# Optimization experiments

Hardware: AMD Instinct MI355X
Metric: run time of the kernel (lower is better)

## Reference

```python
import jax, jax.numpy as jnp
import numpy as np

D_IN = 1024
D_OUT = 1024
NUM_HEADS = 16
HEAD_DIM = D_OUT // NUM_HEADS


def setup_inputs() -> dict:
    key = jax.random.key(0)
    ks = jax.random.split(key, 6)
    s = 0.02
    x = jax.random.normal(ks[0], (2, 2048, D_IN), dtype=jnp.float32)
    wq = jax.random.normal(ks[1], (D_IN, D_OUT), dtype=jnp.float32) * s
    wk = jax.random.normal(ks[2], (D_IN, D_OUT), dtype=jnp.float32) * s
    wv = jax.random.normal(ks[3], (D_IN, D_OUT), dtype=jnp.float32) * s
    wo = jax.random.normal(ks[4], (D_OUT, D_OUT), dtype=jnp.float32) * s
    bo = jax.random.normal(ks[5], (D_OUT,), dtype=jnp.float32) * s
    return {"x": x, "wq": wq, "wk": wk, "wv": wv, "wo": wo, "bo": bo}


def reference(x, wq, wk, wv, wo, bo):
    B, S, _ = x.shape
    # QKV projections (no bias, qkv_bias=False)
    def split_heads(t):
        return t.reshape(B, S, NUM_HEADS, HEAD_DIM).transpose(0, 2, 1, 3)  # [B,H,S,Dh]
    q = split_heads(x @ wq)
    k = split_heads(x @ wk)
    v = split_heads(x @ wv)
    scores = jnp.einsum('bhqd,bhkd->bhqk', q, k) / np.sqrt(HEAD_DIM).astype(np.float32)
    causal = jnp.tril(jnp.ones((S, S), dtype=bool))  # [S,S]
    scores = jnp.where(causal[None, None], scores, -jnp.inf)
    attn = jax.nn.softmax(scores, axis=-1)  # dropout p=0.0 -> identity
    ctx = jnp.einsum('bhqk,bhkd->bhqd', attn, v)
    ctx = ctx.transpose(0, 2, 1, 3).reshape(B, S, D_OUT)
    return ctx @ wo + bo
```

## Files before the change

kernel.cpp:

```cpp
#include <hip/hip_runtime.h>

typedef short s16x8 __attribute__((ext_vector_type(8)));
typedef float f32x4 __attribute__((ext_vector_type(4)));
typedef float f32x16 __attribute__((ext_vector_type(16)));
typedef unsigned int u32;
typedef u32 u32x2 __attribute__((ext_vector_type(2)));
typedef u32 u32x4 __attribute__((ext_vector_type(4)));
typedef unsigned short u16;

#define MFMA16(a, b, c) __builtin_amdgcn_mfma_f32_16x16x32_bf16((a), (b), (c), 0, 0, 0)
#define MFMA32(a, b, c) __builtin_amdgcn_mfma_f32_32x32x16_bf16((a), (b), (c), 0, 0, 0)

__device__ __forceinline__ u16 f2bf(float f) {
  unsigned u = __builtin_bit_cast(unsigned, f);
  unsigned r = (u + 0x7FFFu + ((u >> 16) & 1u)) >> 16;
  return (u16)r;
}

__device__ __forceinline__ u32 pack2bf(float lo, float hi) {
  return (u32)f2bf(lo) | ((u32)f2bf(hi) << 16);
}

__device__ __forceinline__ u32 cvtpk(float lo, float hi) {
  u32 r;
  asm("v_cvt_pk_bf16_f32 %0, %1, %2" : "=v"(r) : "v"(lo), "v"(hi));
  return r;
}

__device__ __forceinline__ float bf2f(u32 lo16) {
  return __builtin_bit_cast(float, lo16 << 16);
}

__device__ __forceinline__ void gl_lds16(const u16* g, u16* s) {
  __builtin_amdgcn_global_load_lds(
      (const __attribute__((address_space(1))) void*)g,
      (__attribute__((address_space(3))) void*)s, 16, 0, 0);
}

__global__ __launch_bounds__(256) void cvt_bf16(const float* __restrict__ in,
                                                u16* __restrict__ out, int n4) {
  int i = blockIdx.x * 256 + threadIdx.x;
  if (i < n4) {
    float4 v = reinterpret_cast<const float4*>(in)[i];
    ushort4 o;
    o.x = f2bf(v.x); o.y = f2bf(v.y); o.z = f2bf(v.z); o.w = f2bf(v.w);
    reinterpret_cast<ushort4*>(out)[i] = o;
  }
}

__global__ __launch_bounds__(256) void transp4(const float* __restrict__ wq,
                                               const float* __restrict__ wk,
                                               const float* __restrict__ wv,
                                               const float* __restrict__ wo,
                                               u16* __restrict__ wqkvt,
                                               u16* __restrict__ wot, float qscale) {
  __shared__ float tile[64][65];
  int z = blockIdx.z;
  const float* W = (z == 0) ? wq : (z == 1) ? wk : (z == 2) ? wv : wo;
  u16* out = (z < 3) ? (wqkvt + z * 1048576) : wot;
  float sc = (z == 0) ? qscale : 1.0f;
  int n0 = blockIdx.x * 64, k0 = blockIdx.y * 64;
  int t = threadIdx.x;
#pragma unroll
  for (int i = 0; i < 16; i++) {
    int idx = t + i * 256;
    int r = idx >> 6, c = idx & 63;
    tile[r][c] = W[(k0 + r) * 1024 + (n0 + c)];
  }
  __syncthreads();
#pragma unroll
  for (int i = 0; i < 16; i++) {
    int idx = t + i * 256;
    int r = idx >> 6, c = idx & 63;
    out[(n0 + r) * 1024 + (k0 + c)] = f2bf(tile[c][r] * sc);
  }
}

template <int MODE>
__global__ __launch_bounds__(256) void gemm2(const u16* __restrict__ A,
                                             const u16* __restrict__ Bt,
                                             const float* __restrict__ bias,
                                             void* __restrict__ outp) {
  constexpr int K = 1024, NT = K / 32;
  __shared__ __align__(16) u16 As[2][128 * 32];
  __shared__ __align__(16) u16 Bs[2][128 * 32];
  int t = threadIdx.x, w = t >> 6, l = t & 63;
  int m0 = blockIdx.y * 128, n0 = blockIdx.x * 128;
  int wm = (w >> 1) * 64, wn = (w & 1) * 64;
  int g = l >> 4, ql = l & 15;

  f32x4 acc[4][4];
#pragma unroll
  for (int i = 0; i < 4; i++)
#pragma unroll
    for (int j = 0; j < 4; j++) acc[i][j] = f32x4{0.f, 0.f, 0.f, 0.f};

  int lrow = l >> 2, lcol = (l & 3) * 8;
  const u16* Ag0 = A + (m0 + 32 * w + lrow) * K + lcol;
  const u16* Bg0 = Bt + (n0 + 32 * w + lrow) * K + lcol;
  u16* Asw[2] = {&As[0][(32 * w) * 32], &As[1][(32 * w) * 32]};
  u16* Bsw[2] = {&Bs[0][(32 * w) * 32], &Bs[1][(32 * w) * 32]};

#define STAGE(buf, kt)                              \
  do {                                              \
    int k0_ = (kt) * 32;                            \
    gl_lds16(Ag0 + k0_, Asw[buf]);                  \
    gl_lds16(Ag0 + 16 * K + k0_, Asw[buf] + 512);   \
    gl_lds16(Bg0 + k0_, Bsw[buf]);                  \
    gl_lds16(Bg0 + 16 * K + k0_, Bsw[buf] + 512);   \
  } while (0)

#define COMPUTE(buf)                                                              \
  do {                                                                            \
    s16x8 af[4], bv[4];                                                           \
    _Pragma("unroll") for (int fm = 0; fm < 4; fm++)                              \
        af[fm] = *reinterpret_cast<const s16x8*>(                                 \
            &As[buf][(wm + fm * 16 + ql) * 32 + g * 8]);                          \
    _Pragma("unroll") for (int fn = 0; fn < 4; fn++)                              \
        bv[fn] = *reinterpret_cast<const s16x8*>(                                 \
            &Bs[buf][(wn + fn * 16 + ql) * 32 + g * 8]);                          \
    _Pragma("unroll") for (int fm = 0; fm < 4; fm++)                              \
        _Pragma("unroll") for (int fn = 0; fn < 4; fn++)                          \
            acc[fm][fn] = MFMA16(af[fm], bv[fn], acc[fm][fn]);                    \
  } while (0)

  STAGE(0, 0);
  __syncthreads();
  int cur = 0;
  for (int kt = 0; kt < NT - 1; kt++) {
    STAGE(cur ^ 1, kt + 1);
    COMPUTE(cur);
    __syncthreads();
    cur ^= 1;
  }
  COMPUTE(cur);
#undef STAGE
#undef COMPUTE

#pragma unroll
  for (int fm = 0; fm < 4; fm++)
#pragma unroll
    for (int fn = 0; fn < 4; fn++)
#pragma unroll
      for (int j = 0; j < 4; j++) {
        int m = m0 + wm + fm * 16 + g * 4 + j;
        int n = n0 + wn + fn * 16 + ql;
        float v = acc[fm][fn][j];
        if (MODE == 0) {
          int proj = n >> 10, nn = n & 1023;
          int bh = (m >> 11) * 16 + (nn >> 6);
          int hd = nn & 63, srow = m & 2047;
          u16* o = (u16*)outp + proj * 4194304;
          if (proj < 2) {
            o[(bh * 2048 + srow) * 64 + hd] = f2bf(v);
          } else {
            int sp = (srow & ~12) | ((srow & 4) << 1) | ((srow & 8) >> 1);
            o[(bh * 64 + hd) * 2048 + sp] = f2bf(v);
          }
        } else {
          ((float*)outp)[m * 1024 + n] = v + bias[n];
        }
      }
}

__global__ __launch_bounds__(512, 4) void attn_kernel(const u16* __restrict__ Q,
                                                      const u16* __restrict__ Kb,
                                                      const u16* __restrict__ Vt,
                                                      u16* __restrict__ Ctx,
                                                      u16* __restrict__ part_o,
                                                      float* __restrict__ part_l) {
  __shared__ __align__(16) u16 Kl[2][2048];
  __shared__ __align__(16) u16 Vl[2][2048];
  __shared__ __align__(16) u16 tl[8][32 * 68];
  int tid = threadIdx.x, w = tid >> 6, l = tid & 63;
  int lq = l & 31, h = l >> 5;

  int B = blockIdx.x;
  int head = (B & 7) + 8 * ((B >> 3) & 3);
  int u = B >> 5;
  const signed char QCv[16] = {3, 2, 4, 4, 6, 6, 6, 7, 7, 7, 7, 5, 5, 5, 1, 0};
  const signed char CKv[16] = {0, 0, 0, 1, 0, 1, 2, 0, 1, 2, 3, 0, 1, 2, 0, 0};
  int qc = QCv[u], ck = CKv[u];
  int t0, t1;
  if (qc == 4)      { t0 = ck * 20; t1 = t0 + 20; }
  else if (qc == 5) { t0 = ck * 16; t1 = t0 + 16; }
  else if (qc == 6) { t0 = (ck == 0) ? 0 : (ck == 1) ? 19 : 38;
                      t1 = (ck == 0) ? 19 : (ck == 1) ? 38 : 56; }
  else if (qc == 7) { t0 = ck * 16; t1 = t0 + 16; }
  else              { t0 = 0; t1 = (qc + 1) * 8; }
  int dtile = qc * 8 + w;
  int q0w = qc * 256 + w * 32;
  int q = q0w + lq;

  const u16* Qp = Q + (head * 2048 + q0w) * 64;
  const u16* Kp = Kb + head * 2048 * 64;
  const u16* Vp = Vt + head * 64 * 2048;

  s16x8 qf[4];
#pragma unroll
  for (int f = 0; f < 4; f++)
    qf[f] = *reinterpret_cast<const s16x8*>(Qp + lq * 64 + f * 16 + h * 8);

  const u16* gstage;
  int gstep, ldsoff;
  if (w < 4) {
    int row = w * 8 + (l >> 3);
    int c = (l & 7) ^ (row & 7);
    gstage = Kp + row * 64 + c * 8;
    gstep = 32 * 64;
    ldsoff = w * 512;
  } else {
    int lin = (w - 4) * 64 + l;
    int rp = lin >> 3, pos = lin & 7;
    int d = rp * 2 + (pos >> 2);
    int c = (pos & 3) ^ (rp & 3);
    gstage = Vp + d * 2048 + c * 8;
    gstep = 32;
    ldsoff = (w - 4) * 512;
  }

  f32x16 oacc[2];
#pragma unroll
  for (int dt = 0; dt < 2; dt++)
#pragma unroll
    for (int rr = 0; rr < 16; rr++) oacc[dt][rr] = 0.f;
  float lsum = 0.f;

#define STAGE(buf, kt)                                                    \
  gl_lds16(gstage + (kt) * gstep, ((w < 4) ? Kl[buf] : Vl[buf]) + ldsoff)

  STAGE(0, t0);
  __syncthreads();
  int cur = 0;

  for (int kt = t0; kt < t1; kt++) {
    if (kt + 1 < t1) STAGE(cur ^ 1, kt + 1);

    if (kt <= dtile) {
      s16x8 kc[4];
#pragma unroll
      for (int f = 0; f < 4; f++)
        kc[f] = *reinterpret_cast<const s16x8*>(
            &Kl[cur][lq * 64 + (((f * 2 + h) ^ (lq & 7)) * 8)]);

      f32x16 s;
#pragma unroll
      for (int rr = 0; rr < 16; rr++) s[rr] = 0.f;
      __builtin_amdgcn_s_setprio(1);
#pragma unroll
      for (int f = 0; f < 4; f++) s = MFMA32(kc[f], qf[f], s);
      __builtin_amdgcn_s_setprio(0);

      float p[16];
      if (kt == dtile) {
        int kb = kt * 32;
#pragma unroll
        for (int rr = 0; rr < 16; rr++) {
          int key = kb + (rr & 3) + 8 * (rr >> 2) + 4 * h;
          float e = exp2f(s[rr]);
          p[rr] = (key <= q) ? e : 0.f;
        }
      } else {
#pragma unroll
        for (int rr = 0; rr < 16; rr++) p[rr] = exp2f(s[rr]);
      }
#pragma unroll
      for (int rr = 0; rr < 16; rr++) lsum += p[rr];

      u32 pw[2][4];
#pragma unroll
      for (int kh = 0; kh < 2; kh++)
#pragma unroll
        for (int uu = 0; uu < 4; uu++)
          pw[kh][uu] = cvtpk(p[kh * 8 + 2 * uu], p[kh * 8 + 2 * uu + 1]);

      s16x8 vf[2][2];
#pragma unroll
      for (int dt = 0; dt < 2; dt++)
#pragma unroll
        for (int kh = 0; kh < 2; kh++) {
          int rp = dt * 16 + (lq >> 1);
          int soff = rp * 64 + (lq & 1) * 32 + (((kh * 2 + h) ^ (rp & 3)) * 8);
          vf[dt][kh] = *reinterpret_cast<const s16x8*>(&Vl[cur][soff]);
        }

      __builtin_amdgcn_s_setprio(1);
#pragma unroll
      for (int kh = 0; kh < 2; kh++) {
        s16x8 pf = __builtin_bit_cast(
            s16x8, u32x4{pw[kh][0], pw[kh][1], pw[kh][2], pw[kh][3]});
        oacc[0] = MFMA32(vf[0][kh], pf, oacc[0]);
        oacc[1] = MFMA32(vf[1][kh], pf, oacc[1]);
      }
      __builtin_amdgcn_s_setprio(0);
    }

    __syncthreads();
    cur ^= 1;
  }
#undef STAGE

  if (qc >= 4) {
    int base = (qc == 4) ? 0 : (qc == 5) ? 2 : (qc == 6) ? 5 : 8;
    int rec = head * 12 + base + ck;
    u32* po = reinterpret_cast<u32*>(part_o) + (size_t)rec * 8192 + w * 1024 + l * 16;
#pragma unroll
    for (int dt = 0; dt < 2; dt++)
#pragma unroll
      for (int i = 0; i < 8; i++)
        po[dt * 8 + i] = pack2bf(oacc[dt][2 * i], oacc[dt][2 * i + 1]);
    part_l[(size_t)rec * 512 + w * 64 + l] = lsum;
    return;
  }

  float ltot = lsum + __shfl_xor(lsum, 32);
  float invl = 1.0f / ltot;
  u16* myl = tl[w];
#pragma unroll
  for (int dt = 0; dt < 2; dt++)
#pragma unroll
    for (int i = 0; i < 8; i++) {
      int d = ((2 * i) & 3) + 8 * (i >> 1) + 4 * h + dt * 32;
      u32 pkv = pack2bf(oacc[dt][2 * i] * invl, oacc[dt][2 * i + 1] * invl);
      *reinterpret_cast<u32*>(myl + lq * 68 + d) = pkv;
    }

  int b = head >> 4, hh = head & 15;
  int gbase = b * 2048 + q0w;
#pragma unroll
  for (int i = 0; i < 8; i++) {
    int chunkk = i * 64 + l;
    int row = chunkk >> 4, col4 = (chunkk & 15) * 4;
    u32x2 v = *reinterpret_cast<const u32x2*>(myl + row * 68 + col4);
    *reinterpret_cast<u32x2*>(Ctx + (gbase + row) * 1024 + hh * 64 + col4) = v;
  }
}

__global__ __launch_bounds__(256) void attn_combine(const u16* __restrict__ part_o,
                                                    const float* __restrict__ part_l,
                                                    u16* __restrict__ Ctx) {
  __shared__ __align__(16) u16 tl[4][32 * 68];
  int wv = threadIdx.x >> 6, l = threadIdx.x & 63;
  int lq = l & 31, h = l >> 5;
  int unit = blockIdx.x * 4 + wv;
  int head = unit & 31, rest = unit >> 5;
  int qc = 4 + (rest >> 3), w = rest & 7;
  int nc = (qc == 4) ? 2 : (qc == 7) ? 4 : 3;
  int base = (qc == 4) ? 0 : (qc == 5) ? 2 : (qc == 6) ? 5 : 8;
  int rec0 = head * 12 + base;

  float lsum = 0.f;
  float of[32];
#pragma unroll
  for (int i = 0; i < 32; i++) of[i] = 0.f;
  for (int cc = 0; cc < nc; cc++) {
    int rec = rec0 + cc;
    lsum += part_l[(size_t)rec * 512 + w * 64 + l];
    const u32* po =
        reinterpret_cast<const u32*>(part_o) + (size_t)rec * 8192 + w * 1024 + l * 16;
#pragma unroll
    for (int uu = 0; uu < 16; uu++) {
      u32 a = po[uu];
      of[2 * uu] += bf2f(a & 0xFFFFu);
      of[2 * uu + 1] += bf2f(a >> 16);
    }
  }

  float ltot = lsum + __shfl_xor(lsum, 32);
  float invl = 1.0f / ltot;

  u16* myl = tl[wv];
#pragma unroll
  for (int dt = 0; dt < 2; dt++)
#pragma unroll
    for (int i = 0; i < 8; i++) {
      int uu = dt * 8 + i;
      int d = ((2 * i) & 3) + 8 * (i >> 1) + 4 * h + dt * 32;
      *reinterpret_cast<u32*>(myl + lq * 68 + d) =
          pack2bf(of[2 * uu] * invl, of[2 * uu + 1] * invl);
    }

  int b_ = head >> 4, hh = head & 15;
  int gbase = b_ * 2048 + qc * 256 + w * 32;
#pragma unroll
  for (int i = 0; i < 8; i++) {
    int chunkk = i * 64 + l;
    int row = chunkk >> 4, col4 = (chunkk & 15) * 4;
    u32x2 v = *reinterpret_cast<const u32x2*>(myl + row * 68 + col4);
    *reinterpret_cast<u32x2*>(Ctx + (gbase + row) * 1024 + hh * 64 + col4) = v;
  }
}

extern "C" void kernel_launch(void* const* d_in, const int* in_sizes, int n_in,
                              void* d_out, int out_size, void* d_ws, size_t ws_size,
                              hipStream_t stream) {
  const float* x = (const float*)d_in[0];
  const float* wq = (const float*)d_in[1];
  const float* wk = (const float*)d_in[2];
  const float* wv = (const float*)d_in[3];
  const float* wo = (const float*)d_in[4];
  const float* bo = (const float*)d_in[5];

  char* ws = (char*)d_ws;
  const size_t MB = 1 << 20;
  u16* xb    = (u16*)(ws + 0 * MB);
  u16* wqkvt = (u16*)(ws + 8 * MB);
  u16* wot   = (u16*)(ws + 14 * MB);
  u16* qkv   = (u16*)(ws + 16 * MB);
  u16* ctx   = (u16*)(ws + 40 * MB);
  u16* part_o   = (u16*)(ws + 0 * MB);
  float* part_l = (float*)(ws + 12582912);

  const float QSCALE = 0.125f * 1.44269504f;

  cvt_bf16<<<4096, 256, 0, stream>>>(x, xb, 1048576);
  transp4<<<dim3(16, 16, 4), 256, 0, stream>>>(wq, wk, wv, wo, wqkvt, wot, QSCALE);

  gemm2<0><<<dim3(24, 32), 256, 0, stream>>>(xb, wqkvt, nullptr, qkv);

  attn_kernel<<<512, 512, 0, stream>>>(qkv, qkv + 4194304, qkv + 8388608, ctx,
                                       part_o, part_l);
  attn_combine<<<256, 256, 0, stream>>>(part_o, part_l, ctx);

  gemm2<1><<<dim3(8, 32), 256, 0, stream>>>(ctx, wot, bo, d_out);
}
```

Measured before the change: 122.1 us.

## Triple-buffer 64-key stages with prefetch depth two in causal attention

Replaces the double-buffered 32-key K/V staging with a triple-buffered ring of 64-key stages, prefetching two stages ahead and waiting with explicit vmcnt counts plus raw s_barrier instead of __syncthreads. Each iteration processes two 32-key subtiles, which halves the number of barriers. The per-block split of key ranges is rebalanced and the block ordering reshuffled, and the shared memory is unified into one buffer that the epilogue staging area aliases. The aim is to hide global-load latency and cut synchronisation overhead, at the cost of more LDS per block (48 KB), which may lower occupancy, and of the fragility of hand-placed waitcnts.

Result: no change. 122.2 us (+0.1%).

```diff
diff --git a/kernel.cpp b/kernel.cpp
--- a/kernel.cpp
+++ b/kernel.cpp
@@ -169,25 +169,18 @@
                                                       u16* __restrict__ Ctx,
                                                       u16* __restrict__ part_o,
                                                       float* __restrict__ part_l) {
-  __shared__ __align__(16) u16 Kl[2][2048];
-  __shared__ __align__(16) u16 Vl[2][2048];
-  __shared__ __align__(16) u16 tl[8][32 * 68];
+  __shared__ __align__(16) u16 shm[24576];
   int tid = threadIdx.x, w = tid >> 6, l = tid & 63;
   int lq = l & 31, h = l >> 5;
 
   int B = blockIdx.x;
   int head = (B & 7) + 8 * ((B >> 3) & 3);
   int u = B >> 5;
-  const signed char QCv[16] = {3, 2, 4, 4, 6, 6, 6, 7, 7, 7, 7, 5, 5, 5, 1, 0};
-  const signed char CKv[16] = {0, 0, 0, 1, 0, 1, 2, 0, 1, 2, 3, 0, 1, 2, 0, 0};
-  int qc = QCv[u], ck = CKv[u];
-  int t0, t1;
-  if (qc == 4)      { t0 = ck * 20; t1 = t0 + 20; }
-  else if (qc == 5) { t0 = ck * 16; t1 = t0 + 16; }
-  else if (qc == 6) { t0 = (ck == 0) ? 0 : (ck == 1) ? 19 : 38;
-                      t1 = (ck == 0) ? 19 : (ck == 1) ? 38 : 56; }
-  else if (qc == 7) { t0 = ck * 16; t1 = t0 + 16; }
-  else              { t0 = 0; t1 = (qc + 1) * 8; }
+  const signed char QCp[16]  = {3, 2, 4, 4, 6, 6, 6, 5, 5, 5, 7, 7, 7, 7, 1, 0};
+  const signed char T0pv[16] = {0, 0, 0, 10, 0, 10, 19, 0, 8, 16, 0, 8, 16, 24, 0, 0};
+  const signed char LENv[16] = {16, 12, 10, 10, 10, 9, 9, 8, 8, 8, 8, 8, 8, 8, 8, 4};
+  const signed char CKv[16]  = {0, 0, 0, 1, 0, 1, 2, 0, 1, 2, 0, 1, 2, 3, 0, 0};
+  int qc = QCp[u], ck = CKv[u], t0p = T0pv[u], n = LENv[u];
   int dtile = qc * 8 + w;
   int q0w = qc * 256 + w * 32;
   int q = q0w + lq;
@@ -201,23 +194,33 @@
   for (int f = 0; f < 4; f++)
     qf[f] = *reinterpret_cast<const s16x8*>(Qp + lq * 64 + f * 16 + h * 8);
 
-  const u16* gstage;
-  int gstep, ldsoff;
+  const u16 *gs0, *gs1;
+  int gstride, lo0, lo1;
   if (w < 4) {
-    int row = w * 8 + (l >> 3);
-    int c = (l & 7) ^ (row & 7);
-    gstage = Kp + row * 64 + c * 8;
-    gstep = 32 * 64;
-    ldsoff = w * 512;
+    int rowa = w * 16 + (l >> 3);
+    gs0 = Kp + rowa * 64 + ((l & 7) ^ (rowa & 7)) * 8;
+    gs1 = gs0 + 512;
+    gstride = 4096;
+    lo0 = w * 1024;
+    lo1 = lo0 + 512;
   } else {
     int lin = (w - 4) * 64 + l;
     int rp = lin >> 3, pos = lin & 7;
     int d = rp * 2 + (pos >> 2);
     int c = (pos & 3) ^ (rp & 3);
-    gstage = Vp + d * 2048 + c * 8;
-    gstep = 32;
-    ldsoff = (w - 4) * 512;
-  }
+    gs0 = Vp + d * 2048 + c * 8;
+    gs1 = gs0 + 32;
+    gstride = 64;
+    lo0 = 4096 + (w - 4) * 512;
+    lo1 = lo0 + 2048;
+  }
+
+#define STAGEP(buf, pi)                          \
+  do {                                           \
+    u16* sb_ = shm + (buf)*8192;                 \
+    gl_lds16(gs0 + (pi)*gstride, sb_ + lo0);     \
+    gl_lds16(gs1 + (pi)*gstride, sb_ + lo1);     \
+  } while (0)
 
   f32x16 oacc[2];
 #pragma unroll
@@ -226,79 +229,96 @@
     for (int rr = 0; rr < 16; rr++) oacc[dt][rr] = 0.f;
   float lsum = 0.f;
 
-#define STAGE(buf, kt)                                                    \
-  gl_lds16(gstage + (kt) * gstep, ((w < 4) ? Kl[buf] : Vl[buf]) + ldsoff)
-
-  STAGE(0, t0);
-  __syncthreads();
+  STAGEP(0, t0p);
+  STAGEP(1, t0p + 1);
+  asm volatile("s_waitcnt vmcnt(2)" ::: "memory");
+  __builtin_amdgcn_sched_barrier(0);
+  __builtin_amdgcn_s_barrier();
+  __builtin_amdgcn_sched_barrier(0);
+
   int cur = 0;
-
-  for (int kt = t0; kt < t1; kt++) {
-    if (kt + 1 < t1) STAGE(cur ^ 1, kt + 1);
-
-    if (kt <= dtile) {
-      s16x8 kc[4];
-#pragma unroll
-      for (int f = 0; f < 4; f++)
-        kc[f] = *reinterpret_cast<const s16x8*>(
-            &Kl[cur][lq * 64 + (((f * 2 + h) ^ (lq & 7)) * 8)]);
-
-      f32x16 s;
-#pragma unroll
-      for (int rr = 0; rr < 16; rr++) s[rr] = 0.f;
-      __builtin_amdgcn_s_setprio(1);
-#pragma unroll
-      for (int f = 0; f < 4; f++) s = MFMA32(kc[f], qf[f], s);
-      __builtin_amdgcn_s_setprio(0);
-
-      float p[16];
-      if (kt == dtile) {
-        int kb = kt * 32;
-#pragma unroll
-        for (int rr = 0; rr < 16; rr++) {
-          int key = kb + (rr & 3) + 8 * (rr >> 2) + 4 * h;
-          float e = exp2f(s[rr]);
-          p[rr] = (key <= q) ? e : 0.f;
+  for (int i = 0; i < n; i++) {
+    u16* sbase = shm + cur * 8192;
+    int tile0 = (t0p + i) * 2;
+
+#pragma unroll
+    for (int sub = 0; sub < 2; sub++) {
+      int kt = tile0 + sub;
+      if (kt <= dtile) {
+        s16x8 kc[4];
+#pragma unroll
+        for (int f = 0; f < 4; f++)
+          kc[f] = *reinterpret_cast<const s16x8*>(
+              &sbase[(sub * 32 + lq) * 64 + (((f * 2 + h) ^ (lq & 7)) * 8)]);
+
+        f32x16 s;
+#pragma unroll
+        for (int rr = 0; rr < 16; rr++) s[rr] = 0.f;
+        __builtin_amdgcn_s_setprio(1);
+#pragma unroll
+        for (int f = 0; f < 4; f++) s = MFMA32(kc[f], qf[f], s);
+        __builtin_amdgcn_s_setprio(0);
+
+        float p[16];
+        if (kt == dtile) {
+          int kb = kt * 32;
+#pragma unroll
+          for (int rr = 0; rr < 16; rr++) {
+            int key = kb + (rr & 3) + 8 * (rr >> 2) + 4 * h;
+            float e = exp2f(s[rr]);
+            p[rr] = (key <= q) ? e : 0.f;
+          }
+        } else {
+#pragma unroll
+          for (int rr = 0; rr < 16; rr++) p[rr] = exp2f(s[rr]);
         }
-      } else {
-#pragma unroll
-        for (int rr = 0; rr < 16; rr++) p[rr] = exp2f(s[rr]);
+#pragma unroll
+        for (int rr = 0; rr < 16; rr++) lsum += p[rr];
+
+        u32 pw[2][4];
+#pragma unroll
+        for (int kh = 0; kh < 2; kh++)
+#pragma unroll
+          for (int uu = 0; uu < 4; uu++)
+            pw[kh][uu] = cvtpk(p[kh * 8 + 2 * uu], p[kh * 8 + 2 * uu + 1]);
+
+        const u16* vb = sbase + 4096 + sub * 2048;
+        s16x8 vf[2][2];
+#pragma unroll
+        for (int dt = 0; dt < 2; dt++)
+#pragma unroll
+          for (int kh = 0; kh < 2; kh++) {
+            int rp = dt * 16 + (lq >> 1);
+            vf[dt][kh] = *reinterpret_cast<const s16x8*>(
+                &vb[rp * 64 + (lq & 1) * 32 + (((kh * 2 + h) ^ (rp & 3)) * 8)]);
+          }
+
+        __builtin_amdgcn_s_setprio(1);
+#pragma unroll
+        for (int kh = 0; kh < 2; kh++) {
+          s16x8 pf = __builtin_bit_cast(
+              s16x8, u32x4{pw[kh][0], pw[kh][1], pw[kh][2], pw[kh][3]});
+          oacc[0] = MFMA32(vf[0][kh], pf, oacc[0]);
+          oacc[1] = MFMA32(vf[1][kh], pf, oacc[1]);
+        }
+        __builtin_amdgcn_s_setprio(0);
       }
-#pragma unroll
-      for (int rr = 0; rr < 16; rr++) lsum += p[rr];
-
-      u32 pw[2][4];
-#pragma unroll
-      for (int kh = 0; kh < 2; kh++)
-#pragma unroll
-        for (int uu = 0; uu < 4; uu++)
-          pw[kh][uu] = cvtpk(p[kh * 8 + 2 * uu], p[kh * 8 + 2 * uu + 1]);
-
-      s16x8 vf[2][2];
-#pragma unroll
-      for (int dt = 0; dt < 2; dt++)
-#pragma unroll
-        for (int kh = 0; kh < 2; kh++) {
-          int rp = dt * 16 + (lq >> 1);
-          int soff = rp * 64 + (lq & 1) * 32 + (((kh * 2 + h) ^ (rp & 3)) * 8);
-          vf[dt][kh] = *reinterpret_cast<const s16x8*>(&Vl[cur][soff]);
-        }
-
-      __builtin_amdgcn_s_setprio(1);
-#pragma unroll
-      for (int kh = 0; kh < 2; kh++) {
-        s16x8 pf = __builtin_bit_cast(
-            s16x8, u32x4{pw[kh][0], pw[kh][1], pw[kh][2], pw[kh][3]});
-        oacc[0] = MFMA32(vf[0][kh], pf, oacc[0]);
-        oacc[1] = MFMA32(vf[1][kh], pf, oacc[1]);
-      }
-      __builtin_amdgcn_s_setprio(0);
     }
 
-    __syncthreads();
-    cur ^= 1;
-  }
-#undef STAGE
+    if (i + 2 < n) {
+      int nb = cur + 2;
+      if (nb >= 3) nb -= 3;
+      STAGEP(nb, t0p + i + 2);
+      asm volatile("s_waitcnt vmcnt(2)" ::: "memory");
+    } else {
+      asm volatile("s_waitcnt vmcnt(0)" ::: "memory");
+    }
+    __builtin_amdgcn_sched_barrier(0);
+    __builtin_amdgcn_s_barrier();
+    __builtin_amdgcn_sched_barrier(0);
+    cur = (cur == 2) ? 0 : cur + 1;
+  }
+#undef STAGEP
 
   if (qc >= 4) {
     int base = (qc == 4) ? 0 : (qc == 5) ? 2 : (qc == 6) ? 5 : 8;
@@ -315,7 +335,7 @@
 
   float ltot = lsum + __shfl_xor(lsum, 32);
   float invl = 1.0f / ltot;
-  u16* myl = tl[w];
+  u16* myl = shm + w * 2176;
 #pragma unroll
   for (int dt = 0; dt < 2; dt++)
 #pragma unroll
```

## Restructure causal attention into 128-row bands with deeper K/V prefetch pipeline

Applied to the files above, without the earlier changes.

The attention kernel moves from 512-thread blocks over 256-query chunks to 256-thread blocks over 128-query bands. A new band/chunk schedule launches 960 blocks, with each block covering at most 24 key tiles. K tiles are staged into a 6-slot LDS ring four tiles ahead. V fragments are loaded straight into registers with inline global loads and explicit vmcnt waits, replacing the V LDS staging and per-tile syncthreads. The aim is better load balance across CUs and more memory latency hidden behind MFMA work, at the cost of more partial records, a larger combine pass, hand-managed wait counts and higher register pressure.

After: 131.1 us. 7.3% more time.

```diff
diff --git a/kernel.cpp b/kernel.cpp
--- a/kernel.cpp
+++ b/kernel.cpp
@@ -36,6 +36,18 @@
       (const __attribute__((address_space(1))) void*)g,
       (__attribute__((address_space(3))) void*)s, 16, 0, 0);
 }
+
+__device__ __forceinline__ u32x4 gload16(const u16* p) {
+  u32x4 r;
+  asm volatile("global_load_dwordx4 %0, %1, off" : "=&v"(r) : "v"(p) : "memory");
+  return r;
+}
+
+#define VMCNT(n)                                             \
+  do {                                                       \
+    asm volatile("s_waitcnt vmcnt(" #n ")" ::: "memory");    \
+    __builtin_amdgcn_sched_barrier(0);                       \
+  } while (0)
 
 __global__ __launch_bounds__(256) void cvt_bf16(const float* __restrict__ in,
                                                 u16* __restrict__ out, int n4) {
@@ -163,61 +175,68 @@
       }
 }
 
-__global__ __launch_bounds__(512, 4) void attn_kernel(const u16* __restrict__ Q,
+__global__ __launch_bounds__(256, 3) void attn_kernel(const u16* __restrict__ Q,
                                                       const u16* __restrict__ Kb,
                                                       const u16* __restrict__ Vt,
                                                       u16* __restrict__ Ctx,
                                                       u16* __restrict__ part_o,
                                                       float* __restrict__ part_l) {
-  __shared__ __align__(16) u16 Kl[2][2048];
-  __shared__ __align__(16) u16 Vl[2][2048];
-  __shared__ __align__(16) u16 tl[8][32 * 68];
+  __shared__ __align__(16) u16 shm[12288];
   int tid = threadIdx.x, w = tid >> 6, l = tid & 63;
   int lq = l & 31, h = l >> 5;
 
   int B = blockIdx.x;
   int head = (B & 7) + 8 * ((B >> 3) & 3);
   int u = B >> 5;
-  const signed char QCv[16] = {3, 2, 4, 4, 6, 6, 6, 7, 7, 7, 7, 5, 5, 5, 1, 0};
-  const signed char CKv[16] = {0, 0, 0, 1, 0, 1, 2, 0, 1, 2, 3, 0, 1, 2, 0, 0};
-  int qc = QCv[u], ck = CKv[u];
-  int t0, t1;
-  if (qc == 4)      { t0 = ck * 20; t1 = t0 + 20; }
-  else if (qc == 5) { t0 = ck * 16; t1 = t0 + 16; }
-  else if (qc == 6) { t0 = (ck == 0) ? 0 : (ck == 1) ? 19 : 38;
-                      t1 = (ck == 0) ? 19 : (ck == 1) ? 38 : 56; }
-  else if (qc == 7) { t0 = ck * 16; t1 = t0 + 16; }
-  else              { t0 = 0; t1 = (qc + 1) * 8; }
-  int dtile = qc * 8 + w;
-  int q0w = qc * 256 + w * 32;
+  const signed char BANDv[30] = {5, 6, 7, 8, 9, 10, 11, 11, 12, 12, 13, 13, 14, 14, 15,
+                                 15, 4, 10, 3, 9, 15, 2, 8, 14, 1, 7, 13, 0, 6, 12};
+  const signed char CKv[30] = {0, 0, 0, 0, 0, 0, 0, 1, 0, 1, 0, 1, 0, 1, 0,
+                               1, 0, 1, 0, 1, 2, 0, 1, 2, 0, 1, 2, 0, 1, 2};
+  int band = BANDv[u], ck = CKv[u];
+  int t0 = ck * 24;
+  int tb = 4 * band + 4;
+  int t1 = (tb < t0 + 24) ? tb : (t0 + 24);
+  int nbody = (t1 - t0) >> 1;
+  int dtile = band * 4 + w;
+  int q0w = band * 128 + w * 32;
   int q = q0w + lq;
 
   const u16* Qp = Q + (head * 2048 + q0w) * 64;
   const u16* Kp = Kb + head * 2048 * 64;
   const u16* Vp = Vt + head * 64 * 2048;
 
+  int krow = w * 8 + (l >> 3);
+  const u16* kgs = Kp + krow * 64 + (((l & 7) ^ (krow & 7)) * 8);
+  int kldso = w * 512;
+
+  const u16* vaddr[4];
+#pragma unroll
+  for (int dt = 0; dt < 2; dt++)
+#pragma unroll
+    for (int kh = 0; kh < 2; kh++)
+      vaddr[dt * 2 + kh] = Vp + (dt * 32 + lq) * 2048 + kh * 16 + h * 8;
+
+#define STAGEK(idx, tile) gl_lds16(kgs + (tile)*2048, shm + (idx)*2048 + kldso)
+
+  u32x4 qfr[4];
+#pragma unroll
+  for (int f = 0; f < 4; f++) qfr[f] = gload16(Qp + lq * 64 + f * 16 + h * 8);
+  STAGEK(0, t0);
+  STAGEK(1, t0 + 1);
+  STAGEK(2, t0 + 2);
+  STAGEK(3, t0 + 3);
+  u32x4 VA[4], VB[4];
+#pragma unroll
+  for (int x = 0; x < 4; x++) VA[x] = gload16(vaddr[x] + t0 * 32);
+#pragma unroll
+  for (int x = 0; x < 4; x++) VB[x] = gload16(vaddr[x] + t0 * 32 + 32);
+  VMCNT(10);
+  __builtin_amdgcn_s_barrier();
+  __builtin_amdgcn_sched_barrier(0);
+
   s16x8 qf[4];
 #pragma unroll
-  for (int f = 0; f < 4; f++)
-    qf[f] = *reinterpret_cast<const s16x8*>(Qp + lq * 64 + f * 16 + h * 8);
-
-  const u16* gstage;
-  int gstep, ldsoff;
-  if (w < 4) {
-    int row = w * 8 + (l >> 3);
-    int c = (l & 7) ^ (row & 7);
-    gstage = Kp + row * 64 + c * 8;
-    gstep = 32 * 64;
-    ldsoff = w * 512;
-  } else {
-    int lin = (w - 4) * 64 + l;
-    int rp = lin >> 3, pos = lin & 7;
-    int d = rp * 2 + (pos >> 2);
-    int c = (pos & 3) ^ (rp & 3);
-    gstage = Vp + d * 2048 + c * 8;
-    gstep = 32;
-    ldsoff = (w - 4) * 512;
-  }
+  for (int f = 0; f < 4; f++) qf[f] = __builtin_bit_cast(s16x8, qfr[f]);
 
   f32x16 oacc[2];
 #pragma unroll
@@ -226,96 +245,95 @@
     for (int rr = 0; rr < 16; rr++) oacc[dt][rr] = 0.f;
   float lsum = 0.f;
 
-#define STAGE(buf, kt)                                                    \
-  gl_lds16(gstage + (kt) * gstep, ((w < 4) ? Kl[buf] : Vl[buf]) + ldsoff)
-
-  STAGE(0, t0);
-  __syncthreads();
-  int cur = 0;
-
-  for (int kt = t0; kt < t1; kt++) {
-    if (kt + 1 < t1) STAGE(cur ^ 1, kt + 1);
-
-    if (kt <= dtile) {
-      s16x8 kc[4];
-#pragma unroll
-      for (int f = 0; f < 4; f++)
-        kc[f] = *reinterpret_cast<const s16x8*>(
-            &Kl[cur][lq * 64 + (((f * 2 + h) ^ (lq & 7)) * 8)]);
-
-      f32x16 s;
-#pragma unroll
-      for (int rr = 0; rr < 16; rr++) s[rr] = 0.f;
-      __builtin_amdgcn_s_setprio(1);
-#pragma unroll
-      for (int f = 0; f < 4; f++) s = MFMA32(kc[f], qf[f], s);
-      __builtin_amdgcn_s_setprio(0);
-
-      float p[16];
-      if (kt == dtile) {
-        int kb = kt * 32;
-#pragma unroll
-        for (int rr = 0; rr < 16; rr++) {
-          int key = kb + (rr & 3) + 8 * (rr >> 2) + 4 * h;
-          float e = exp2f(s[rr]);
-          p[rr] = (key <= q) ? e : 0.f;
-        }
-      } else {
-#pragma unroll
-        for (int rr = 0; rr < 16; rr++) p[rr] = exp2f(s[rr]);
-      }
-#pragma unroll
-      for (int rr = 0; rr < 16; rr++) lsum += p[rr];
-
-      u32 pw[2][4];
-#pragma unroll
-      for (int kh = 0; kh < 2; kh++)
-#pragma unroll
-        for (int uu = 0; uu < 4; uu++)
-          pw[kh][uu] = cvtpk(p[kh * 8 + 2 * uu], p[kh * 8 + 2 * uu + 1]);
-
-      s16x8 vf[2][2];
-#pragma unroll
-      for (int dt = 0; dt < 2; dt++)
-#pragma unroll
-        for (int kh = 0; kh < 2; kh++) {
-          int rp = dt * 16 + (lq >> 1);
-          int soff = rp * 64 + (lq & 1) * 32 + (((kh * 2 + h) ^ (rp & 3)) * 8);
-          vf[dt][kh] = *reinterpret_cast<const s16x8*>(&Vl[cur][soff]);
-        }
-
-      __builtin_amdgcn_s_setprio(1);
-#pragma unroll
-      for (int kh = 0; kh < 2; kh++) {
-        s16x8 pf = __builtin_bit_cast(
-            s16x8, u32x4{pw[kh][0], pw[kh][1], pw[kh][2], pw[kh][3]});
-        oacc[0] = MFMA32(vf[0][kh], pf, oacc[0]);
-        oacc[1] = MFMA32(vf[1][kh], pf, oacc[1]);
-      }
-      __builtin_amdgcn_s_setprio(0);
+#define TILE_COMPUTE(KT, BUFI, VREG, MIDWAIT)                                     \
+  do {                                                                            \
+    int kt_ = (KT);                                                               \
+    if (kt_ <= dtile) {                                                           \
+      const u16* kb_ = shm + (BUFI)*2048;                                         \
+      s16x8 kc[4];                                                                \
+      _Pragma("unroll") for (int f = 0; f < 4; f++)                               \
+          kc[f] = *reinterpret_cast<const s16x8*>(                                \
+              &kb_[lq * 64 + (((f * 2 + h) ^ (lq & 7)) * 8)]);                    \
+      f32x16 s;                                                                   \
+      _Pragma("unroll") for (int rr = 0; rr < 16; rr++) s[rr] = 0.f;              \
+      __builtin_amdgcn_s_setprio(1);                                              \
+      _Pragma("unroll") for (int f = 0; f < 4; f++) s = MFMA32(kc[f], qf[f], s);  \
+      __builtin_amdgcn_s_setprio(0);                                              \
+      float p[16];                                                                \
+      if (kt_ == dtile) {                                                         \
+        int kb0_ = kt_ * 32;                                                      \
+        _Pragma("unroll") for (int rr = 0; rr < 16; rr++) {                       \
+          int key = kb0_ + (rr & 3) + 8 * (rr >> 2) + 4 * h;                      \
+          float e = exp2f(s[rr]);                                                 \
+          p[rr] = (key <= q) ? e : 0.f;                                           \
+        }                                                                         \
+      } else {                                                                    \
+        _Pragma("unroll") for (int rr = 0; rr < 16; rr++) p[rr] = exp2f(s[rr]);   \
+      }                                                                           \
+      _Pragma("unroll") for (int rr = 0; rr < 16; rr++) lsum += p[rr];            \
+      u32 pw[2][4];                                                               \
+      _Pragma("unroll") for (int kh = 0; kh < 2; kh++)                            \
+          _Pragma("unroll") for (int uu = 0; uu < 4; uu++)                        \
+              pw[kh][uu] = cvtpk(p[kh * 8 + 2 * uu], p[kh * 8 + 2 * uu + 1]);     \
+      MIDWAIT;                                                                    \
+      __builtin_amdgcn_s_setprio(1);                                              \
+      _Pragma("unroll") for (int kh = 0; kh < 2; kh++) {                          \
+        s16x8 pf = __builtin_bit_cast(                                            \
+            s16x8, u32x4{pw[kh][0], pw[kh][1], pw[kh][2], pw[kh][3]});            \
+        oacc[0] = MFMA32(__builtin_bit_cast(s16x8, VREG[0 * 2 + kh]), pf, oacc[0]); \
+        oacc[1] = MFMA32(__builtin_bit_cast(s16x8, VREG[1 * 2 + kh]), pf, oacc[1]); \
+      }                                                                           \
+      __builtin_amdgcn_s_setprio(0);                                              \
+    }                                                                             \
+  } while (0)
+
+  int bi = 0;
+  for (int j = 0; j < nbody; j++) {
+    int kt = t0 + 2 * j;
+
+    TILE_COMPUTE(kt, bi, VA, VMCNT(4));
+    TILE_COMPUTE(kt + 1, bi + 1, VB, VMCNT(0));
+
+    bool moreV = (kt + 2 < t1);
+    bool moreK = (kt + 4 < t1);
+    int s0 = (bi >= 2) ? (bi - 2) : (bi + 4);
+    if (moreK) {
+      STAGEK(s0, kt + 4);
+      STAGEK(s0 + 1, kt + 5);
     }
-
-    __syncthreads();
-    cur ^= 1;
-  }
-#undef STAGE
-
-  if (qc >= 4) {
-    int base = (qc == 4) ? 0 : (qc == 5) ? 2 : (qc == 6) ? 5 : 8;
-    int rec = head * 12 + base + ck;
-    u32* po = reinterpret_cast<u32*>(part_o) + (size_t)rec * 8192 + w * 1024 + l * 16;
+    if (moreV) {
+#pragma unroll
+      for (int x = 0; x < 4; x++) VA[x] = gload16(vaddr[x] + (kt + 2) * 32);
+#pragma unroll
+      for (int x = 0; x < 4; x++) VB[x] = gload16(vaddr[x] + (kt + 3) * 32);
+      VMCNT(10);
+    } else {
+      VMCNT(0);
+    }
+    __builtin_amdgcn_s_barrier();
+    __builtin_amdgcn_sched_barrier(0);
+    bi += 2;
+    if (bi >= 6) bi -= 6;
+  }
+#undef TILE_COMPUTE
+#undef STAGEK
+
+  if (band >= 6) {
+    int base = (band <= 11) ? (band - 6) * 2 : 12 + (band - 12) * 3;
+    int rec = head * 24 + base + ck;
+    u32* po = reinterpret_cast<u32*>(part_o) + (size_t)rec * 4096 + w * 1024 + l * 16;
 #pragma unroll
     for (int dt = 0; dt < 2; dt++)
 #pragma unroll
       for (int i = 0; i < 8; i++)
         po[dt * 8 + i] = pack2bf(oacc[dt][2 * i], oacc[dt][2 * i + 1]);
-    part_l[(size_t)rec * 512 + w * 64 + l] = lsum;
+    part_l[(size_t)rec * 256 + w * 64 + l] = lsum;
     return;
   }
 
   float ltot = lsum + __shfl_xor(lsum, 32);
   float invl = 1.0f / ltot;
-  u16* myl = tl[w];
+  u16* myl = shm + w * 2176;
 #pragma unroll
   for (int dt = 0; dt < 2; dt++)
 #pragma unroll
@@ -344,10 +362,10 @@
   int lq = l & 31, h = l >> 5;
   int unit = blockIdx.x * 4 + wv;
   int head = unit & 31, rest = unit >> 5;
-  int qc = 4 + (rest >> 3), w = rest & 7;
-  int nc = (qc == 4) ? 2 : (qc == 7) ? 4 : 3;
-  int base = (qc == 4) ? 0 : (qc == 5) ? 2 : (qc == 6) ? 5 : 8;
-  int rec0 = head * 12 + base;
+  int band = 6 + (rest >> 2), w = rest & 3;
+  int nc = (band <= 11) ? 2 : 3;
+  int base = (band <= 11) ? (band - 6) * 2 : 12 + (band - 12) * 3;
+  int rec0 = head * 24 + base;
 
   float lsum = 0.f;
   float of[32];
@@ -355,9 +373,9 @@
   for (int i = 0; i < 32; i++) of[i] = 0.f;
   for (int cc = 0; cc < nc; cc++) {
     int rec = rec0 + cc;
-    lsum += part_l[(size_t)rec * 512 + w * 64 + l];
+    lsum += part_l[(size_t)rec * 256 + w * 64 + l];
     const u32* po =
-        reinterpret_cast<const u32*>(part_o) + (size_t)rec * 8192 + w * 1024 + l * 16;
+        reinterpret_cast<const u32*>(part_o) + (size_t)rec * 4096 + w * 1024 + l * 16;
 #pragma unroll
     for (int uu = 0; uu < 16; uu++) {
       u32 a = po[uu];
@@ -381,7 +399,7 @@
     }
 
   int b_ = head >> 4, hh = head & 15;
-  int gbase = b_ * 2048 + qc * 256 + w * 32;
+  int gbase = b_ * 2048 + band * 128 + w * 32;
 #pragma unroll
   for (int i = 0; i < 8; i++) {
     int chunkk = i * 64 + l;
@@ -418,9 +436,9 @@
 
   gemm2<0><<<dim3(24, 32), 256, 0, stream>>>(xb, wqkvt, nullptr, qkv);
 
-  attn_kernel<<<512, 512, 0, stream>>>(qkv, qkv + 4194304, qkv + 8388608, ctx,
+  attn_kernel<<<960, 256, 0, stream>>>(qkv, qkv + 4194304, qkv + 8388608, ctx,
                                        part_o, part_l);
-  attn_combine<<<256, 256, 0, stream>>>(part_o, part_l, ctx);
+  attn_combine<<<320, 256, 0, stream>>>(part_o, part_l, ctx);
 
   gemm2<1><<<dim3(8, 32), 256, 0, stream>>>(ctx, wot, bo, d_out);
 }
```

## Replace QKV projection GEMM with 256x128-tile, 8-wave, triple-buffered pipelined kernel

Applied to the files above, without the earlier changes.

Adds a new QKV projection kernel that uses 256x128 output tiles with 512 threads and a three-slot LDS ring. Global-to-LDS loads are issued two stages ahead, with explicit vmcnt/lgkmcnt waits, split A/B staging interleaved with the MFMA groups, and one barrier per k-step. The aim is to hide global load latency better and raise data reuse per block than the old double-buffered 128x128 kernel. The old templated GEMM is specialized to the output projection only. The trade-off is more LDS per block and hand-tuned wait counts that must match the number of loads in flight.

New measurement: 124.4 us. About the same (+1.9%).

```diff
diff --git a/kernel.cpp b/kernel.cpp
--- a/kernel.cpp
+++ b/kernel.cpp
@@ -36,6 +36,18 @@
       (const __attribute__((address_space(1))) void*)g,
       (__attribute__((address_space(3))) void*)s, 16, 0, 0);
 }
+
+#define VMCNT(n)                                             \
+  do {                                                       \
+    asm volatile("s_waitcnt vmcnt(" #n ")" ::: "memory");    \
+    __builtin_amdgcn_sched_barrier(0);                       \
+  } while (0)
+
+#define LGKM0                                                \
+  do {                                                       \
+    asm volatile("s_waitcnt lgkmcnt(0)" ::: "memory");       \
+    __builtin_amdgcn_sched_barrier(0);                       \
+  } while (0)
 
 __global__ __launch_bounds__(256) void cvt_bf16(const float* __restrict__ in,
                                                 u16* __restrict__ out, int n4) {
@@ -76,11 +88,119 @@
   }
 }
 
-template <int MODE>
+__global__ __launch_bounds__(512, 4) void gemm8(const u16* __restrict__ A,
+                                                const u16* __restrict__ Bt,
+                                                void* __restrict__ outp) {
+  __shared__ __align__(16) u16 shm[36864];
+  int t = threadIdx.x, w = t >> 6, l = t & 63;
+  int ql = l & 15, g = l >> 4;
+  int m0 = blockIdx.y * 256, n0 = blockIdx.x * 128;
+  int wm64 = (w >> 1) * 64;
+  int wn64 = (w & 1) * 64;
+  int xs = ((g ^ (l & 3)) * 8);
+
+  int r0 = w * 16 + (l >> 2);
+  int c0 = (l & 3) ^ (r0 & 3);
+  const u16* pA0 = A + (m0 + r0) * 1024 + c0 * 8;
+  const u16* pB0 = Bt + (n0 + r0) * 1024 + c0 * 8;
+  int w512 = w * 512;
+
+  f32x4 acc[4][4];
+#pragma unroll
+  for (int i = 0; i < 4; i++)
+#pragma unroll
+    for (int j = 0; j < 4; j++) acc[i][j] = f32x4{0.f, 0.f, 0.f, 0.f};
+
+#define STAGE_A(slot, s)                                        \
+  do {                                                          \
+    u16* d_ = shm + (slot)*12288 + w512;                        \
+    gl_lds16(pA0 + (s)*32, d_);                                 \
+    gl_lds16(pA0 + 131072 + (s)*32, d_ + 4096);                 \
+  } while (0)
+#define STAGE_B(slot, s) gl_lds16(pB0 + (s)*32, shm + (slot)*12288 + 8192 + w512)
+
+  STAGE_A(0, 0);
+  STAGE_B(0, 0);
+  STAGE_A(1, 1);
+  STAGE_B(1, 1);
+  VMCNT(3);
+  __builtin_amdgcn_s_barrier();
+  __builtin_amdgcn_sched_barrier(0);
+
+  int r = 0;
+  for (int s = 0; s < 32; ++s) {
+    const u16* As_ = shm + r * 12288;
+    const u16* Bs_ = As_ + 8192;
+    int r2 = r - 1;
+    if (r2 < 0) r2 = 2;
+    bool st = (s < 30);
+
+    s16x8 af0 = *reinterpret_cast<const s16x8*>(As_ + (wm64 + 0 + ql) * 32 + xs);
+    s16x8 af1 = *reinterpret_cast<const s16x8*>(As_ + (wm64 + 16 + ql) * 32 + xs);
+    s16x8 bv[4];
+#pragma unroll
+    for (int fn = 0; fn < 4; fn++)
+      bv[fn] = *reinterpret_cast<const s16x8*>(Bs_ + (wn64 + fn * 16 + ql) * 32 + xs);
+    if (st) STAGE_A(r2, s + 2);
+    LGKM0;
+    __builtin_amdgcn_s_setprio(1);
+#pragma unroll
+    for (int fn = 0; fn < 4; fn++) acc[0][fn] = MFMA16(af0, bv[fn], acc[0][fn]);
+#pragma unroll
+    for (int fn = 0; fn < 4; fn++) acc[1][fn] = MFMA16(af1, bv[fn], acc[1][fn]);
+    __builtin_amdgcn_s_setprio(0);
+
+    s16x8 af2 = *reinterpret_cast<const s16x8*>(As_ + (wm64 + 32 + ql) * 32 + xs);
+    s16x8 af3 = *reinterpret_cast<const s16x8*>(As_ + (wm64 + 48 + ql) * 32 + xs);
+    if (st) STAGE_B(r2, s + 2);
+    LGKM0;
+    __builtin_amdgcn_s_setprio(1);
+#pragma unroll
+    for (int fn = 0; fn < 4; fn++) acc[2][fn] = MFMA16(af2, bv[fn], acc[2][fn]);
+#pragma unroll
+    for (int fn = 0; fn < 4; fn++) acc[3][fn] = MFMA16(af3, bv[fn], acc[3][fn]);
+    __builtin_amdgcn_s_setprio(0);
+
+    if (st) {
+      VMCNT(3);
+    } else if (s == 30) {
+      VMCNT(0);
+    }
+    if (s < 31) {
+      __builtin_amdgcn_s_barrier();
+      __builtin_amdgcn_sched_barrier(0);
+    }
+    r = (r == 2) ? 0 : r + 1;
+  }
+#undef STAGE_A
+#undef STAGE_B
+
+#pragma unroll
+  for (int fm = 0; fm < 4; fm++)
+#pragma unroll
+    for (int fn = 0; fn < 4; fn++)
+#pragma unroll
+      for (int j = 0; j < 4; j++) {
+        int m = m0 + wm64 + fm * 16 + g * 4 + j;
+        int n = n0 + wn64 + fn * 16 + ql;
+        float v = acc[fm][fn][j];
+        int proj = n >> 10, nn = n & 1023;
+        int bh = (m >> 11) * 16 + (nn >> 6);
+        int hd = nn & 63, srow = m & 2047;
+        u16* o = (u16*)outp + proj * 4194304;
+        if (proj < 2) {
+          o[(bh * 2048 + srow) * 64 + hd] = f2bf(v);
+        } else {
+          int sp = (srow & ~12) | ((srow & 4) << 1) | ((srow & 8) >> 1);
+          o[(bh * 64 + hd) * 2048 + sp] = f2bf(v);
+        }
+      }
+}
+
 __global__ __launch_bounds__(256) void gemm2(const u16* __restrict__ A,
                                              const u16* __restrict__ Bt,
                                              const float* __restrict__ bias,
-                                             void* __restrict__ outp) {
+                                             float* __restrict__ outp) {
   constexpr int K = 1024, NT = K / 32;
   __shared__ __align__(16) u16 As[2][128 * 32];
   __shared__ __align__(16) u16 Bs[2][128 * 32];
@@ -145,21 +265,7 @@
       for (int j = 0; j < 4; j++) {
         int m = m0 + wm + fm * 16 + g * 4 + j;
         int n = n0 + wn + fn * 16 + ql;
-        float v = acc[fm][fn][j];
-        if (MODE == 0) {
-          int proj = n >> 10, nn = n & 1023;
-          int bh = (m >> 11) * 16 + (nn >> 6);
-          int hd = nn & 63, srow = m & 2047;
-          u16* o = (u16*)outp + proj * 4194304;
-          if (proj < 2) {
-            o[(bh * 2048 + srow) * 64 + hd] = f2bf(v);
-          } else {
-            int sp = (srow & ~12) | ((srow & 4) << 1) | ((srow & 8) >> 1);
-            o[(bh * 64 + hd) * 2048 + sp] = f2bf(v);
-          }
-        } else {
-          ((float*)outp)[m * 1024 + n] = v + bias[n];
-        }
+        outp[m * 1024 + n] = acc[fm][fn][j] + bias[n];
       }
 }
 
@@ -226,15 +332,15 @@
     for (int rr = 0; rr < 16; rr++) oacc[dt][rr] = 0.f;
   float lsum = 0.f;
 
-#define STAGE(buf, kt)                                                    \
+#define STAGEKV(buf, kt)                                                  \
   gl_lds16(gstage + (kt) * gstep, ((w < 4) ? Kl[buf] : Vl[buf]) + ldsoff)
 
-  STAGE(0, t0);
+  STAGEKV(0, t0);
   __syncthreads();
   int cur = 0;
 
   for (int kt = t0; kt < t1; kt++) {
-    if (kt + 1 < t1) STAGE(cur ^ 1, kt + 1);
+    if (kt + 1 < t1) STAGEKV(cur ^ 1, kt + 1);
 
     if (kt <= dtile) {
       s16x8 kc[4];
@@ -298,7 +404,7 @@
     __syncthreads();
     cur ^= 1;
   }
-#undef STAGE
+#undef STAGEKV
 
   if (qc >= 4) {
     int base = (qc == 4) ? 0 : (qc == 5) ? 2 : (qc == 6) ? 5 : 8;
@@ -416,11 +522,11 @@
   cvt_bf16<<<4096, 256, 0, stream>>>(x, xb, 1048576);
   transp4<<<dim3(16, 16, 4), 256, 0, stream>>>(wq, wk, wv, wo, wqkvt, wot, QSCALE);
 
-  gemm2<0><<<dim3(24, 32), 256, 0, stream>>>(xb, wqkvt, nullptr, qkv);
+  gemm8<<<dim3(24, 16), 512, 0, stream>>>(xb, wqkvt, qkv);
 
   attn_kernel<<<512, 512, 0, stream>>>(qkv, qkv + 4194304, qkv + 8388608, ctx,
                                        part_o, part_l);
   attn_combine<<<256, 256, 0, stream>>>(part_o, part_l, ctx);
 
-  gemm2<1><<<dim3(8, 32), 256, 0, stream>>>(ctx, wot, bo, d_out);
-}
+  gemm2<<<dim3(8, 32), 256, 0, stream>>>(ctx, wot, bo, (float*)d_out);
+}
```
